# Performance work log

Hardware: AMD Instinct MI355X
Metric: run time of the kernel (lower is better)

The kernel has to match this reference:

```python
import jax, jax.numpy as jnp
import numpy as np

B, L, V, H = 2, 2048, 1024, 16
HD = V // H  # head size 64
EPS = 1e-3   # keras LayerNormalization default


def setup_inputs() -> dict:
    key = jax.random.key(0)
    ks = jax.random.split(key, 10)
    scale = 1.0 / np.sqrt(V)
    return {
        "query": jax.random.normal(ks[0], (B, L, V), jnp.float32),
        "key_t": jax.random.normal(ks[1], (B, L, V), jnp.float32),
        "value": jax.random.normal(ks[2], (B, L, V), jnp.float32),
        "Wq": jax.random.normal(ks[3], (H, V, HD), jnp.float32) * scale,
        "Wk": jax.random.normal(ks[4], (H, V, HD), jnp.float32) * scale,
        "Wv": jax.random.normal(ks[5], (H, V, HD), jnp.float32) * scale,
        "gamma": jnp.ones((V,), jnp.float32),
        "beta": jnp.zeros((V,), jnp.float32),
        "query_mask": jax.random.randint(ks[6], (B, L), 0, 2, jnp.int32),
        "value_mask": jax.random.randint(ks[7], (B, L), 0, 2, jnp.int32),
    }


def reference(query, key_t, value, Wq, Wk, Wv, gamma, beta, query_mask, value_mask):
    qm = query_mask.astype(jnp.float32)  # (B,L)
    vm = value_mask.astype(jnp.float32)  # (B,L)

    # per-head no-bias Dense projections, batched over heads
    Q = jnp.einsum('blv,hvd->bhld', query, Wq)
    K = jnp.einsum('blv,hvd->bhld', key_t, Wk)
    Vh = jnp.einsum('blv,hvd->bhld', value, Wv)

    scores = jnp.einsum('bhld,bhmd->bhlm', Q, K) / jnp.sqrt(jnp.float32(HD))
    attn = jax.nn.softmax(scores, axis=-1)

    # post-softmax multiplicative masking (faithful to original)
    tri = jnp.tril(jnp.ones((L, L), jnp.float32))  # (L,L) causal
    attn = attn * tri[None, None, :, :]
    attn = attn * qm[:, None, :, None] * vm[:, None, None, :]

    heads = jnp.einsum('bhlm,bhmd->bhld', attn, Vh)
    x = heads.transpose(0, 2, 1, 3).reshape(B, L, V)  # concat heads

    # dropout is identity at inference
    y = x + query
    mu = jnp.mean(y, axis=-1, keepdims=True)
    var = jnp.mean((y - mu) ** 2, axis=-1, keepdims=True)
    return gamma * (y - mu) * jax.lax.rsqrt(var + EPS) + beta
```

## Files before the change

### kernel.cpp

```cpp
#include <hip/hip_runtime.h>
#include <math.h>

constexpr int NB = 2;
constexpr int SL = 2048;
constexpr int NV = 1024;
constexpr int NH = 16;
constexpr int DH = 64;
constexpr float LN_EPS = 1e-3f;

typedef __bf16 bf16_t;
typedef __bf16 v8bf __attribute__((ext_vector_type(8)));
typedef float  v4f  __attribute__((ext_vector_type(4)));

__device__ __forceinline__ unsigned pack_bf16(float a, float b) {
  unsigned short ua = __builtin_bit_cast(unsigned short, (bf16_t)a);
  unsigned short ub = __builtin_bit_cast(unsigned short, (bf16_t)b);
  return (unsigned)ua | ((unsigned)ub << 16);
}
__device__ __forceinline__ void async_cp16(const void* g, void* l) {
  __builtin_amdgcn_global_load_lds(
      (const __attribute__((address_space(1))) unsigned int*)g,
      (__attribute__((address_space(3))) unsigned int*)l, 16, 0, 0);
}
__device__ __forceinline__ void drain_dma() {
  asm volatile("s_waitcnt vmcnt(0)" ::: "memory");
}

__global__ __launch_bounds__(256)
void acvt(const float* __restrict__ q, const float* __restrict__ k,
          const float* __restrict__ v, bf16_t* __restrict__ oq,
          bf16_t* __restrict__ ok, bf16_t* __restrict__ ov) {
  const int z = blockIdx.y;
  const float* src = z == 0 ? q : (z == 1 ? k : v);
  bf16_t*      dst = z == 0 ? oq : (z == 1 ? ok : ov);
  const size_t i = ((size_t)blockIdx.x * 256 + threadIdx.x) * 4;
  float4 f = *(const float4*)(src + i);
  uint2 u = {pack_bf16(f.x, f.y), pack_bf16(f.z, f.w)};
  *(uint2*)(dst + i) = u;
}

__global__ __launch_bounds__(256)
void wcvt(const float* __restrict__ Wq, const float* __restrict__ Wk,
          const float* __restrict__ Wv, bf16_t* __restrict__ Wt) {
  __shared__ float ls[64][65];
  const int z = blockIdx.z;
  const float* W = z == 0 ? Wq : (z == 1 ? Wk : Wv);
  const float sc = z == 0 ? 0.125f * 1.44269504f : 1.0f;
  const int h = blockIdx.y, v0 = blockIdx.x * 64;
  const int t = threadIdx.x;
  const int rr = t >> 4, c4 = t & 15;
  const float* src = W + ((size_t)h * NV + v0) * DH;
#pragma unroll
  for (int it = 0; it < 4; ++it) {
    float4 f = *(const float4*)(src + (size_t)(rr + it * 16) * DH + c4 * 4);
    ls[rr + it * 16][c4 * 4 + 0] = f.x;
    ls[rr + it * 16][c4 * 4 + 1] = f.y;
    ls[rr + it * 16][c4 * 4 + 2] = f.z;
    ls[rr + it * 16][c4 * 4 + 3] = f.w;
  }
  __syncthreads();
  const int dd = t >> 2, vq = t & 3;
  bf16_t tmp[16];
#pragma unroll
  for (int i = 0; i < 16; ++i) tmp[i] = (bf16_t)(ls[vq * 16 + i][dd] * sc);
  bf16_t* dst = Wt + ((size_t)z * NV + h * 64 + dd) * NV + v0 + vq * 16;
  *(v8bf*)dst = *(v8bf*)&tmp[0];
  *(v8bf*)(dst + 8) = *(v8bf*)&tmp[8];
}

__global__ __launch_bounds__(256, 4)
void proj_mfma(const bf16_t* __restrict__ A0, const bf16_t* __restrict__ A1,
               const bf16_t* __restrict__ A2, const bf16_t* __restrict__ Wtb,
               const int* __restrict__ vmask,
               bf16_t* __restrict__ O0, bf16_t* __restrict__ O1,
               bf16_t* __restrict__ O2) {
  __shared__ __align__(16) bf16_t Asb[2][128 * 32];
  __shared__ __align__(16) bf16_t Wsb[2][128 * 32];

  const int z = blockIdx.z;
  const bf16_t* A   = z == 0 ? A0 : (z == 1 ? A1 : A2);
  bf16_t*       out = z == 0 ? O0 : (z == 1 ? O1 : O2);
  const bf16_t* W   = Wtb + (size_t)z * NV * NV;

  const int t = threadIdx.x, w = t >> 6, lane = t & 63;
  const int g = lane >> 4, lx = lane & 15;
  const int m0 = blockIdx.x * 128, n0 = blockIdx.y * 128;
  const int rbase = (w >> 1) * 64, cbase = (w & 1) * 64;

  const int sr = lane >> 2;
  const int sc = (lane & 3);
  auto stageA = [&](int k0, int buf) {
#pragma unroll
    for (int s = 0; s < 2; ++s) {
      const int r = w * 32 + s * 16 + sr;
      const int c = sc ^ (r & 3);
      async_cp16(A + (size_t)(m0 + r) * NV + k0 + c * 8,
                 (char*)Asb[buf] + (w * 32 + s * 16) * 64);
    }
  };
  auto stageW = [&](int k0, int buf) {
#pragma unroll
    for (int s = 0; s < 2; ++s) {
      const int r = w * 32 + s * 16 + sr;
      const int c = sc ^ (r & 3);
      async_cp16(W + (size_t)(n0 + r) * NV + k0 + c * 8,
                 (char*)Wsb[buf] + (w * 32 + s * 16) * 64);
    }
  };

  v4f acc[4][4] = {};
  stageA(0, 0);
  stageW(0, 0);

  for (int it = 0; it < 32; ++it) {
    const int buf = it & 1;
    drain_dma();
    __syncthreads();
    if (it < 31) {
      stageA((it + 1) * 32, buf ^ 1);
      stageW((it + 1) * 32, buf ^ 1);
    }
    v8bf af[4], wf[4];
#pragma unroll
    for (int rt = 0; rt < 4; ++rt) {
      const int row = rbase + rt * 16 + lx;
      af[rt] = *(const v8bf*)((const char*)Asb[buf] + row * 64 +
                              ((g ^ (row & 3)) * 16));
    }
#pragma unroll
    for (int ct = 0; ct < 4; ++ct) {
      const int row = cbase + ct * 16 + lx;
      wf[ct] = *(const v8bf*)((const char*)Wsb[buf] + row * 64 +
                              ((g ^ (row & 3)) * 16));
    }
#pragma unroll
    for (int rt = 0; rt < 4; ++rt)
#pragma unroll
      for (int ct = 0; ct < 4; ++ct)
        acc[rt][ct] = __builtin_amdgcn_mfma_f32_16x16x32_bf16(
            af[rt], wf[ct], acc[rt][ct], 0, 0, 0);
  }

  if (z < 2) {
#pragma unroll
    for (int rt = 0; rt < 4; ++rt) {
#pragma unroll
      for (int reg = 0; reg < 4; ++reg) {
        const int row = m0 + rbase + rt * 16 + g * 4 + reg;
        const int b = row >> 11, l = row & (SL - 1);
#pragma unroll
        for (int ct = 0; ct < 4; ++ct) {
          const int n = n0 + cbase + ct * 16 + lx;
          const int h = n >> 6, d = n & 63;
          out[((size_t)(b * NH + h) * SL + l) * DH + d] = (bf16_t)acc[rt][ct][reg];
        }
      }
    }
  } else {
#pragma unroll
    for (int rt = 0; rt < 4; ++rt) {
      const int row = m0 + rbase + rt * 16 + g * 4;
      const int b = row >> 11, l = row & (SL - 1);
      float vm0 = (float)vmask[b * SL + l + 0];
      float vm1 = (float)vmask[b * SL + l + 1];
      float vm2 = (float)vmask[b * SL + l + 2];
      float vm3 = (float)vmask[b * SL + l + 3];
#pragma unroll
      for (int ct = 0; ct < 4; ++ct) {
        const int n = n0 + cbase + ct * 16 + lx;
        const int h = n >> 6, d = n & 63;
        uint2 u = {pack_bf16(acc[rt][ct][0] * vm0, acc[rt][ct][1] * vm1),
                   pack_bf16(acc[rt][ct][2] * vm2, acc[rt][ct][3] * vm3)};
        *(uint2*)&out[((size_t)(b * NH + h) * DH + d) * SL + l] = u;
      }
    }
  }
}

__global__ __launch_bounds__(256, 4)
void attn_mfma(const bf16_t* __restrict__ Qg, const bf16_t* __restrict__ Kg,
               const bf16_t* __restrict__ Vtg_all, const int* __restrict__ qmask,
               float* __restrict__ Xout) {
  __shared__ __align__(16) char smem[16896];
  bf16_t* Ps   = (bf16_t*)smem;
  float*  obuf = (float*)smem;
  float*  sbuf = (float*)(smem + 16384);

  const int id = blockIdx.x;
  const int bh = (id & 7) | ((id >> 8) << 3);
  const int qraw = (id >> 3) & 31;
  const int qb = ((id >> 8) & 1) ? qraw : 31 - qraw;
  const int t = threadIdx.x, w = t >> 6, lane = t & 63;
  const int wq = w & 1, wm = w >> 1;
  const int g = lane >> 4, lx = lane & 15;
  const int b = bh >> 4, h = bh & 15;
  const int l0 = qb * 64;
  const int lastAct = qb;

  const bf16_t* Kb  = Kg + (size_t)bh * SL * DH;
  const bf16_t* Vtg = Vtg_all + (size_t)bh * DH * SL;

  v8bf qf[2][2];
#pragma unroll
  for (int qt = 0; qt < 2; ++qt)
#pragma unroll
    for (int ks = 0; ks < 2; ++ks)
      qf[qt][ks] = *(const v8bf*)&Qg[((size_t)bh * SL + l0 + wq * 32 + qt * 16 + lx) * DH +
                                     ks * 32 + g * 8];

  v4f O[2][4] = {};
  float suml[2] = {0.f, 0.f};

  for (int mt = 0; mt <= lastAct; ++mt) {
    const int mb = mt * 64;
    v4f S[2][2];
#pragma unroll
    for (int mt2 = 0; mt2 < 2; ++mt2) {
      S[mt2][0] = (v4f){0.f, 0.f, 0.f, 0.f};
      S[mt2][1] = (v4f){0.f, 0.f, 0.f, 0.f};
    }
#pragma unroll
    for (int ks = 0; ks < 2; ++ks)
#pragma unroll
      for (int mt2 = 0; mt2 < 2; ++mt2) {
        v8bf kf = *(const v8bf*)&Kb[(size_t)(mb + wm * 32 + mt2 * 16 + lx) * DH +
                                    ks * 32 + g * 8];
#pragma unroll
        for (int qt = 0; qt < 2; ++qt)
          S[mt2][qt] = __builtin_amdgcn_mfma_f32_16x16x32_bf16(
              kf, qf[qt][ks], S[mt2][qt], 0, 0, 0);
      }

    const bool diagzone = (mt == qb);
#pragma unroll
    for (int mt2 = 0; mt2 < 2; ++mt2)
#pragma unroll
      for (int qt = 0; qt < 2; ++qt) {
        float e0 = __builtin_amdgcn_exp2f(S[mt2][qt][0]);
        float e1 = __builtin_amdgcn_exp2f(S[mt2][qt][1]);
        float e2 = __builtin_amdgcn_exp2f(S[mt2][qt][2]);
        float e3 = __builtin_amdgcn_exp2f(S[mt2][qt][3]);
        suml[qt] += (e0 + e1) + (e2 + e3);
        if (diagzone) {
          const int ml = mb + wm * 32 + mt2 * 16 + g * 4;
          const int ql = l0 + wq * 32 + qt * 16 + lx;
          e0 = (ml + 0 <= ql) ? e0 : 0.f;
          e1 = (ml + 1 <= ql) ? e1 : 0.f;
          e2 = (ml + 2 <= ql) ? e2 : 0.f;
          e3 = (ml + 3 <= ql) ? e3 : 0.f;
        }
        uint2 u = {pack_bf16(e0, e1), pack_bf16(e2, e3)};
        *(uint2*)((char*)&Ps[w * 1024] + (qt * 16 + lx) * 64 +
                  (((mt2 * 2 + (g >> 1)) ^ ((lx >> 1) & 3)) * 16) +
                  (g & 1) * 8) = u;
      }

    __builtin_amdgcn_wave_barrier();

    v8bf pf[2];
#pragma unroll
    for (int qt = 0; qt < 2; ++qt)
      pf[qt] = *(const v8bf*)((const char*)&Ps[w * 1024] + (qt * 16 + lx) * 64 +
                              ((g ^ ((lx >> 1) & 3)) * 16));
#pragma unroll
    for (int dt = 0; dt < 4; ++dt) {
      v8bf vf = *(const v8bf*)&Vtg[(size_t)(dt * 16 + lx) * SL + mb +
                                   wm * 32 + g * 8];
#pragma unroll
      for (int qt = 0; qt < 2; ++qt)
        O[qt][dt] = __builtin_amdgcn_mfma_f32_16x16x32_bf16(
            pf[qt], vf, O[qt][dt], 0, 0, 0);
    }
  }

  for (int mt = lastAct + 1; mt < SL / 64; ++mt) {
    const int mb = mt * 64;
    v4f S[2][2];
#pragma unroll
    for (int mt2 = 0; mt2 < 2; ++mt2) {
      S[mt2][0] = (v4f){0.f, 0.f, 0.f, 0.f};
      S[mt2][1] = (v4f){0.f, 0.f, 0.f, 0.f};
    }
#pragma unroll
    for (int ks = 0; ks < 2; ++ks)
#pragma unroll
      for (int mt2 = 0; mt2 < 2; ++mt2) {
        v8bf kf = *(const v8bf*)&Kb[(size_t)(mb + wm * 32 + mt2 * 16 + lx) * DH +
                                    ks * 32 + g * 8];
#pragma unroll
        for (int qt = 0; qt < 2; ++qt)
          S[mt2][qt] = __builtin_amdgcn_mfma_f32_16x16x32_bf16(
              kf, qf[qt][ks], S[mt2][qt], 0, 0, 0);
      }
#pragma unroll
    for (int mt2 = 0; mt2 < 2; ++mt2)
#pragma unroll
      for (int qt = 0; qt < 2; ++qt)
        suml[qt] += (__builtin_amdgcn_exp2f(S[mt2][qt][0]) +
                     __builtin_amdgcn_exp2f(S[mt2][qt][1])) +
                    (__builtin_amdgcn_exp2f(S[mt2][qt][2]) +
                     __builtin_amdgcn_exp2f(S[mt2][qt][3]));
  }

  suml[0] += __shfl_xor(suml[0], 16); suml[0] += __shfl_xor(suml[0], 32);
  suml[1] += __shfl_xor(suml[1], 16); suml[1] += __shfl_xor(suml[1], 32);

  __syncthreads();
  if (g == 0) {
    sbuf[((wq * 2 + wm) * 2 + 0) * 16 + lx] = suml[0];
    sbuf[((wq * 2 + wm) * 2 + 1) * 16 + lx] = suml[1];
  }
  if (wm == 1) {
#pragma unroll
    for (int qt = 0; qt < 2; ++qt)
#pragma unroll
      for (int dt = 0; dt < 4; ++dt)
#pragma unroll
        for (int reg = 0; reg < 4; ++reg)
          obuf[wq * 2048 + (qt * 16 + g * 4 + reg) * 64 +
               ((dt * 16 + lx) ^ ((g & 1) * 16))] = O[qt][dt][reg];
  }
  __syncthreads();
  if (wm == 0) {
#pragma unroll
    for (int qt = 0; qt < 2; ++qt) {
      const float stot = suml[qt] + sbuf[((wq * 2 + 1) * 2 + qt) * 16 + lx];
#pragma unroll
      for (int reg = 0; reg < 4; ++reg) {
        const int q = l0 + wq * 32 + qt * 16 + g * 4 + reg;
        const float den = __shfl(stot, g * 4 + reg);
        const float inv = (float)qmask[b * SL + q] / den;
#pragma unroll
        for (int dt = 0; dt < 4; ++dt) {
          const float val =
              (O[qt][dt][reg] +
               obuf[wq * 2048 + (qt * 16 + g * 4 + reg) * 64 +
                    ((dt * 16 + lx) ^ ((g & 1) * 16))]) *
              inv;
          Xout[((size_t)(b * SL + q)) * NV + h * DH + dt * 16 + lx] = val;
        }
      }
    }
  }
}

__global__ __launch_bounds__(256)
void ln_kernel(const float* __restrict__ X, const float* __restrict__ query,
               const float* __restrict__ gamma, const float* __restrict__ beta,
               float* __restrict__ out) {
  const int row = blockIdx.x * 4 + (threadIdx.x >> 6);
  const int lane = threadIdx.x & 63;
  const float* xr = X + (size_t)row * NV;
  const float* qr = query + (size_t)row * NV;
  float4 y[4];
  float s = 0.f, ss = 0.f;
#pragma unroll
  for (int i = 0; i < 4; ++i) {
    const int col = lane * 4 + i * 256;
    float4 xv = *(const float4*)(xr + col);
    float4 qv = *(const float4*)(qr + col);
    y[i].x = xv.x + qv.x; y[i].y = xv.y + qv.y;
    y[i].z = xv.z + qv.z; y[i].w = xv.w + qv.w;
    s  += (y[i].x + y[i].y) + (y[i].z + y[i].w);
    ss += (y[i].x * y[i].x + y[i].y * y[i].y) +
          (y[i].z * y[i].z + y[i].w * y[i].w);
  }
#pragma unroll
  for (int off = 1; off < 64; off <<= 1) {
    s  += __shfl_xor(s, off);
    ss += __shfl_xor(ss, off);
  }
  const float mu   = s * (1.f / NV);
  const float var  = ss * (1.f / NV) - mu * mu;
  const float rstd = rsqrtf(var + LN_EPS);
#pragma unroll
  for (int i = 0; i < 4; ++i) {
    const int col = lane * 4 + i * 256;
    float4 gv = *(const float4*)(gamma + col);
    float4 bv = *(const float4*)(beta + col);
    float4 o;
    o.x = gv.x * (y[i].x - mu) * rstd + bv.x;
    o.y = gv.y * (y[i].y - mu) * rstd + bv.y;
    o.z = gv.z * (y[i].z - mu) * rstd + bv.z;
    o.w = gv.w * (y[i].w - mu) * rstd + bv.w;
    *(float4*)(out + (size_t)row * NV + col) = o;
  }
}

extern "C" void kernel_launch(void* const* d_in, const int* in_sizes, int n_in,
                              void* d_out, int out_size, void* d_ws, size_t ws_size,
                              hipStream_t stream) {
  const float* query = (const float*)d_in[0];
  const float* key_t = (const float*)d_in[1];
  const float* value = (const float*)d_in[2];
  const float* Wq    = (const float*)d_in[3];
  const float* Wk    = (const float*)d_in[4];
  const float* Wv    = (const float*)d_in[5];
  const float* gamma = (const float*)d_in[6];
  const float* beta  = (const float*)d_in[7];
  const int*   qmask = (const int*)d_in[8];
  const int*   vmask = (const int*)d_in[9];
  float* out = (float*)d_out;

  const size_t per = (size_t)NB * NH * SL * DH;
  bf16_t* Qws = (bf16_t*)d_ws;
  bf16_t* Kws = Qws + per;
  bf16_t* Vws = Kws + per;
  bf16_t* Wtb = Vws + per;
  bf16_t* Aq  = Wtb + (size_t)3 * NV * NV;
  bf16_t* Ak  = Aq + per;
  bf16_t* Av  = Ak + per;

  acvt<<<dim3((NB * SL * NV) / (256 * 4), 3), 256, 0, stream>>>(
      query, key_t, value, Aq, Ak, Av);
  wcvt<<<dim3(16, 16, 3), 256, 0, stream>>>(Wq, Wk, Wv, Wtb);
  proj_mfma<<<dim3(32, 8, 3), 256, 0, stream>>>(Aq, Ak, Av, Wtb,
                                                vmask, Qws, Kws, Vws);
  attn_mfma<<<1024, 256, 0, stream>>>(Qws, Kws, Vws, qmask, out);
  ln_kernel<<<NB * SL / 4, 256, 0, stream>>>(out, query, gamma, beta, out);
}
```

Measured before the change: 246.7 us.

## Double-buffer K and V tiles in LDS with async global-to-LDS prefetch

The attention kernel now stages each wave's K and V^T tiles into swizzled, double-buffered LDS regions using global_load_lds DMA. The next tile is prefetched while the current one is computed, with explicit vmcnt waits. This is meant to hide global-memory latency on the K/V operand loads that were previously read straight from global memory inside the MFMA loop. In exchange LDS use grows from about 17KB to 72KB per block and launch bounds drop from 4 to 2 blocks per CU, which cuts occupancy. The per-wave waits also rely on careful vmcnt counting.

```diff
diff --git a/kernel.cpp b/kernel.cpp
--- a/kernel.cpp
+++ b/kernel.cpp
@@ -177,14 +177,11 @@
   }
 }
 
-__global__ __launch_bounds__(256, 4)
+__global__ __launch_bounds__(256, 2)
 void attn_mfma(const bf16_t* __restrict__ Qg, const bf16_t* __restrict__ Kg,
                const bf16_t* __restrict__ Vtg_all, const int* __restrict__ qmask,
                float* __restrict__ Xout) {
-  __shared__ __align__(16) char smem[16896];
-  bf16_t* Ps   = (bf16_t*)smem;
-  float*  obuf = (float*)smem;
-  float*  sbuf = (float*)(smem + 16384);
+  __shared__ __align__(16) char smem[73728];
 
   const int id = blockIdx.x;
   const int bh = (id & 7) | ((id >> 8) << 3);
@@ -196,6 +193,13 @@
   const int b = bh >> 4, h = bh & 15;
   const int l0 = qb * 64;
   const int lastAct = qb;
+  const int NT = SL / 64;
+
+  char* kw = smem + w * 8192;
+  char* vw = smem + 32768 + w * 8192;
+  char* Pw = smem + 65536 + w * 2048;
+  float* obuf = (float*)smem;
+  float* sbuf = (float*)(smem + 16384);
 
   const bf16_t* Kb  = Kg + (size_t)bh * SL * DH;
   const bf16_t* Vtg = Vtg_all + (size_t)bh * DH * SL;
@@ -211,8 +215,40 @@
   v4f O[2][4] = {};
   float suml[2] = {0.f, 0.f};
 
+  const int sr8 = lane >> 3, sc8 = lane & 7;
+  auto stageK = [&](int mb, int buf) {
+#pragma unroll
+    for (int s = 0; s < 4; ++s) {
+      const int r = s * 8 + sr8;
+      const int c = sc8 ^ (r & 7);
+      async_cp16(Kb + (size_t)(mb + wm * 32 + r) * DH + c * 8,
+                 kw + buf * 4096 + s * 1024);
+    }
+  };
+  const int sr4 = lane >> 2, sc4 = lane & 3;
+  auto stageV = [&](int mb, int buf) {
+#pragma unroll
+    for (int s = 0; s < 4; ++s) {
+      const int r = s * 16 + sr4;
+      const int c = sc4 ^ ((r >> 1) & 3);
+      async_cp16(Vtg + (size_t)r * SL + mb + wm * 32 + c * 8,
+                 vw + buf * 4096 + s * 1024);
+    }
+  };
+
+  stageK(0, 0);
+  stageV(0, 0);
+
   for (int mt = 0; mt <= lastAct; ++mt) {
-    const int mb = mt * 64;
+    const int pb = mt & 1;
+    const bool nk = (mt + 1 < NT);
+    const bool nv = (mt + 1 <= lastAct);
+    if (nk) stageK((mt + 1) * 64, pb ^ 1);
+    if (nv) stageV((mt + 1) * 64, pb ^ 1);
+    if (nk && nv)      asm volatile("s_waitcnt vmcnt(8)" ::: "memory");
+    else if (nk)       asm volatile("s_waitcnt vmcnt(4)" ::: "memory");
+    else               asm volatile("s_waitcnt vmcnt(0)" ::: "memory");
+
     v4f S[2][2];
 #pragma unroll
     for (int mt2 = 0; mt2 < 2; ++mt2) {
@@ -223,8 +259,9 @@
     for (int ks = 0; ks < 2; ++ks)
 #pragma unroll
       for (int mt2 = 0; mt2 < 2; ++mt2) {
-        v8bf kf = *(const v8bf*)&Kb[(size_t)(mb + wm * 32 + mt2 * 16 + lx) * DH +
-                                    ks * 32 + g * 8];
+        const int lr = mt2 * 16 + lx;
+        v8bf kf = *(const v8bf*)(kw + pb * 4096 + lr * 128 +
+                                 (((ks * 4 + g) ^ (lx & 7)) * 16));
 #pragma unroll
         for (int qt = 0; qt < 2; ++qt)
           S[mt2][qt] = __builtin_amdgcn_mfma_f32_16x16x32_bf16(
@@ -242,7 +279,7 @@
         float e3 = __builtin_amdgcn_exp2f(S[mt2][qt][3]);
         suml[qt] += (e0 + e1) + (e2 + e3);
         if (diagzone) {
-          const int ml = mb + wm * 32 + mt2 * 16 + g * 4;
+          const int ml = mt * 64 + wm * 32 + mt2 * 16 + g * 4;
           const int ql = l0 + wq * 32 + qt * 16 + lx;
           e0 = (ml + 0 <= ql) ? e0 : 0.f;
           e1 = (ml + 1 <= ql) ? e1 : 0.f;
@@ -250,7 +287,7 @@
           e3 = (ml + 3 <= ql) ? e3 : 0.f;
         }
         uint2 u = {pack_bf16(e0, e1), pack_bf16(e2, e3)};
-        *(uint2*)((char*)&Ps[w * 1024] + (qt * 16 + lx) * 64 +
+        *(uint2*)(Pw + (qt * 16 + lx) * 64 +
                   (((mt2 * 2 + (g >> 1)) ^ ((lx >> 1) & 3)) * 16) +
                   (g & 1) * 8) = u;
       }
@@ -260,12 +297,13 @@
     v8bf pf[2];
 #pragma unroll
     for (int qt = 0; qt < 2; ++qt)
-      pf[qt] = *(const v8bf*)((const char*)&Ps[w * 1024] + (qt * 16 + lx) * 64 +
+      pf[qt] = *(const v8bf*)(Pw + (qt * 16 + lx) * 64 +
                               ((g ^ ((lx >> 1) & 3)) * 16));
 #pragma unroll
     for (int dt = 0; dt < 4; ++dt) {
-      v8bf vf = *(const v8bf*)&Vtg[(size_t)(dt * 16 + lx) * SL + mb +
-                                   wm * 32 + g * 8];
+      const int r = dt * 16 + lx;
+      v8bf vf = *(const v8bf*)(vw + pb * 4096 + r * 64 +
+                               ((g ^ ((lx >> 1) & 3)) * 16));
 #pragma unroll
       for (int qt = 0; qt < 2; ++qt)
         O[qt][dt] = __builtin_amdgcn_mfma_f32_16x16x32_bf16(
@@ -273,8 +311,15 @@
     }
   }
 
-  for (int mt = lastAct + 1; mt < SL / 64; ++mt) {
-    const int mb = mt * 64;
+  for (int mt = lastAct + 1; mt < NT; ++mt) {
+    const int pb = mt & 1;
+    const bool nk = (mt + 1 < NT);
+    if (nk) {
+      stageK((mt + 1) * 64, pb ^ 1);
+      asm volatile("s_waitcnt vmcnt(4)" ::: "memory");
+    } else {
+      asm volatile("s_waitcnt vmcnt(0)" ::: "memory");
+    }
     v4f S[2][2];
 #pragma unroll
     for (int mt2 = 0; mt2 < 2; ++mt2) {
@@ -285,8 +330,9 @@
     for (int ks = 0; ks < 2; ++ks)
 #pragma unroll
       for (int mt2 = 0; mt2 < 2; ++mt2) {
-        v8bf kf = *(const v8bf*)&Kb[(size_t)(mb + wm * 32 + mt2 * 16 + lx) * DH +
-                                    ks * 32 + g * 8];
+        const int lr = mt2 * 16 + lx;
+        v8bf kf = *(const v8bf*)(kw + pb * 4096 + lr * 128 +
+                                 (((ks * 4 + g) ^ (lx & 7)) * 16));
 #pragma unroll
         for (int qt = 0; qt < 2; ++qt)
           S[mt2][qt] = __builtin_amdgcn_mfma_f32_16x16x32_bf16(
```

Measured after the change: 221.5 us. -10.2%, faster.
